# Kernel optimization log

Measured on AMD Instinct MI355X. Metric: run time of the kernel, lower is better.

The kernel has to match this reference:

```python
import jax, jax.numpy as jnp
import numpy as np
from jax import lax

N, C, H, W = 6, 64, 128, 128
BN_EPS = 1e-5


def setup_inputs() -> dict:
    key = jax.random.key(0)
    ks = jax.random.split(key, 16)
    def p(i, shape, scale=0.05):
        return jax.random.normal(ks[i], shape, jnp.float32) * scale
    return {
        "raw_feat": jax.random.normal(ks[0], (N, C, H, W), jnp.float32),
        # PixelWeightedFusionSoftmax params (1x1 convs stored as [out,in] matrices)
        "pw_w1": p(1, (4, C)), "pw_b1": p(2, (4,)),
        "bn_gamma": 1.0 + p(3, (4,)), "bn_beta": p(4, (4,)),
        "bn_mean": jnp.zeros((4,), jnp.float32), "bn_var": jnp.ones((4,), jnp.float32),
        "pw_w2": p(5, (1, 4)), "pw_b2": p(6, (1,)),
        # ConvMod params: a = dwconv11x11(gelu(conv1x1_{2C->C}(q))); out = proj(a * v(v) * att_map)
        "cm_a1_w": p(7, (C, 2 * C)), "cm_a1_b": p(8, (C,)),
        "cm_dw_w": p(9, (C, 1, 11, 11)), "cm_dw_b": p(10, (C,)),
        "cm_v_w": p(11, (C, C)), "cm_v_b": p(12, (C,)),
        "cm_proj_w": p(13, (C, C)), "cm_proj_b": p(14, (C,)),
    }


def _conf_maps(x, pw_w1, pw_b1, bn_gamma, bn_beta, bn_mean, bn_var, pw_w2, pw_b2):
    # x: [N,C,H,W] -> per-agent confidence maps [N,1,H,W], min-max normalized per agent
    h = jnp.einsum('nchw,oc->nohw', x, pw_w1) + pw_b1[:, None, None]
    scale = (bn_gamma / jnp.sqrt(bn_var + BN_EPS))[:, None, None]
    h = (h - bn_mean[:, None, None]) * scale + bn_beta[:, None, None]  # BN eval mode
    h = jax.nn.relu(h)
    h = jax.nn.relu(jnp.einsum('nchw,oc->nohw', h, pw_w2) + pw_b2[:, None, None])
    mn = h.min(axis=(1, 2, 3), keepdims=True)
    mx = h.max(axis=(1, 2, 3), keepdims=True)
    return (h - mn) / (mx - mn)


def reference(raw_feat, pw_w1, pw_b1, bn_gamma, bn_beta, bn_mean, bn_var, pw_w2, pw_b2,
              cm_a1_w, cm_a1_b, cm_dw_w, cm_dw_b, cm_v_w, cm_v_b, cm_proj_w, cm_proj_b):
    conf = _conf_maps(raw_feat, pw_w1, pw_b1, bn_gamma, bn_beta, bn_mean, bn_var, pw_w2, pw_b2)  # [N,1,H,W]
    # att_map[i,k] = (1 - conf_i) * conf_k
    att_map = (1.0 - conf)[:, None] * conf[None, :]  # [N,N,1,H,W]
    # q[i,k] = concat(raw[i], raw[k]) along channels -> [N,N,2C,H,W]
    q = jnp.concatenate([jnp.broadcast_to(raw_feat[:, None], (N, N, C, H, W)),
                         jnp.broadcast_to(raw_feat[None, :], (N, N, C, H, W))], axis=2)
    a = jax.nn.gelu(jnp.einsum('ikchw,oc->ikohw', q, cm_a1_w) + cm_a1_b[:, None, None],
                    approximate=False)
    a = lax.conv_general_dilated(a.reshape(N * N, C, H, W), cm_dw_w,
                                 window_strides=(1, 1), padding='SAME',
                                 feature_group_count=C,
                                 dimension_numbers=('NCHW', 'OIHW', 'NCHW'))
    a = a.reshape(N, N, C, H, W) + cm_dw_b[:, None, None]
    vproj = jnp.einsum('nchw,oc->nohw', raw_feat, cm_v_w) + cm_v_b[:, None, None]  # [N,C,H,W]
    x = a * vproj[None] * att_map  # [N,N,C,H,W]
    out = jnp.einsum('ikchw,oc->ikohw', x, cm_proj_w) + cm_proj_b[:, None, None]
    updated = raw_feat + out.sum(axis=1)  # ego i accumulates over all senders k
    return updated.reshape(N * C, H, W)   # matches torch.cat(local_com_mat_update, dim=0)
```

## Files before the change

kernel.cpp:

```cpp
#include <hip/hip_runtime.h>
#include <hip/hip_fp16.h>
#include <math.h>

#define NAG 6
#define CC  64
#define HH  128
#define WW  128
#define HWT 16384
#define HWP 8192
#define BN_EPS 1e-5f
#define WFRAG_PJ_OFF (24 * 64 * 8)

typedef unsigned int u32;
typedef __fp16 f16x2v __attribute__((ext_vector_type(2)));
typedef __fp16 f16x8  __attribute__((ext_vector_type(8)));
typedef float  f32x4  __attribute__((ext_vector_type(4)));

__device__ __forceinline__ u32 gelu_pk(u32 xu) {
    __half2 x = __builtin_bit_cast(__half2, xu);
    __half2 s = __hmul2(x, x);
    __half2 m = __hfma2(s, __float2half2_rn(-0.10294535f),
                        __float2half2_rn(-2.30226045f));
    __half2 e = h2exp2(__hmul2(x, m));
    __half2 r = h2rcp(__hadd2(e, __float2half2_rn(1.0f)));
    return __builtin_bit_cast(u32, __hmul2(x, r));
}

__global__ __launch_bounds__(256) void k_setup(
    const float* __restrict__ a1w, const float* __restrict__ vw,
    const float* __restrict__ pjw, __fp16* __restrict__ wfrag,
    u32* __restrict__ mm)
{
    int t = blockIdx.x * 256 + threadIdx.x;
    if (t < NAG) mm[t] = 0x7F800000u;
    else if (t < 2 * NAG && t >= NAG) mm[t] = 0u;
    if (t >= 32 * 64) return;
    int lane = t & 63;
    int slot = t >> 6;
    bool pj = slot >= 24;
    int s = pj ? slot - 24 : slot;
    int ot = s >> 1, kf = s & 1;
    int o  = (pj ? ot : (ot & 3)) * 16 + (lane & 15);
    int ch = kf * 32 + (lane >> 4) * 8;
    const float* src;
    if (pj)          src = pjw + o * CC + ch;
    else if (ot < 4) src = a1w + o * 2 * CC + ch;
    else if (ot < 8) src = a1w + o * 2 * CC + CC + ch;
    else             src = vw  + o * CC + ch;
    __fp16* dst = wfrag + ((size_t)slot * 64 + lane) * 8;
    #pragma unroll
    for (int j = 0; j < 8; ++j) dst[j] = (__fp16)src[j];
}

__global__ __launch_bounds__(256) void k_conf(
    const float* __restrict__ raw,
    const float* __restrict__ w1, const float* __restrict__ b1,
    const float* __restrict__ gamma, const float* __restrict__ beta,
    const float* __restrict__ mean, const float* __restrict__ var,
    const float* __restrict__ w2, const float* __restrict__ b2,
    float* __restrict__ conf, u32* __restrict__ mm)
{
    const int n = blockIdx.y;
    const int p = blockIdx.x * 256 + threadIdx.x;
    const float* x = raw + (size_t)(n * CC) * HWT + p;

    float a[4] = {0.f, 0.f, 0.f, 0.f};
    #pragma unroll 8
    for (int c = 0; c < CC; ++c) {
        float v = x[c * HWT];
        a[0] = fmaf(w1[0 * CC + c], v, a[0]);
        a[1] = fmaf(w1[1 * CC + c], v, a[1]);
        a[2] = fmaf(w1[2 * CC + c], v, a[2]);
        a[3] = fmaf(w1[3 * CC + c], v, a[3]);
    }
    float h2 = b2[0];
    #pragma unroll
    for (int o = 0; o < 4; ++o) {
        float sc = gamma[o] * rsqrtf(var[o] + BN_EPS);
        float hb = (a[o] + b1[o] - mean[o]) * sc + beta[o];
        hb = fmaxf(hb, 0.f);
        h2 = fmaf(w2[o], hb, h2);
    }
    h2 = fmaxf(h2, 0.f);
    conf[n * HWT + p] = h2;

    float mn = h2, mx = h2;
    #pragma unroll
    for (int off = 32; off > 0; off >>= 1) {
        mn = fminf(mn, __shfl_xor(mn, off, 64));
        mx = fmaxf(mx, __shfl_xor(mx, off, 64));
    }
    __shared__ float smn[4], smx[4];
    int wid = threadIdx.x >> 6, lane = threadIdx.x & 63;
    if (lane == 0) { smn[wid] = mn; smx[wid] = mx; }
    __syncthreads();
    if (threadIdx.x == 0) {
        mn = fminf(fminf(smn[0], smn[1]), fminf(smn[2], smn[3]));
        mx = fmaxf(fmaxf(smx[0], smx[1]), fmaxf(smx[2], smx[3]));
        atomicMin(&mm[n], __float_as_uint(mn));
        atomicMax(&mm[n + NAG], __float_as_uint(mx));
    }
}

__global__ __launch_bounds__(256) void k_pqv(
    const float* __restrict__ raw, const __fp16* __restrict__ wfrag,
    const float* __restrict__ vb, const float* __restrict__ conf,
    const u32* __restrict__ mm,
    u32* __restrict__ Ph, u32* __restrict__ Qh, u32* __restrict__ Wh)
{
    const int n   = blockIdx.y;
    const int px0 = blockIdx.x * 128;
    const int t = threadIdx.x, lane = t & 63, wv = t >> 6;
    const int lm = lane & 15, kg = lane >> 4;
    const int pxw = px0 + wv * 32;
    const int pxl = pxw + lm;
    const int pxs = pxw + kg * 4;

    const float* rawn = raw + (size_t)n * CC * HWT;

    f16x8 afr[2][2];
    #pragma unroll
    for (int mt = 0; mt < 2; ++mt) {
        #pragma unroll
        for (int kf = 0; kf < 2; ++kf) {
            const float* base = rawn + (size_t)(kf * 32 + kg * 8) * HWT + pxl + mt * 16;
            f16x8 a;
            #pragma unroll
            for (int p = 0; p < 4; ++p) {
                f16x2v h = __builtin_amdgcn_cvt_pkrtz(base[(2 * p) * HWT],
                                                      base[(2 * p + 1) * HWT]);
                a[2 * p] = h.x; a[2 * p + 1] = h.y;
            }
            afr[mt][kf] = a;
        }
    }

    const float mn = __uint_as_float(mm[n]);
    const float mx = __uint_as_float(mm[n + NAG]);
    const float inv = 1.f / (mx - mn);
    f32x4 cn[2];
    #pragma unroll
    for (int mt = 0; mt < 2; ++mt) {
        f32x4 cv = *(const f32x4*)(conf + n * HWT + pxs + mt * 16);
        cn[mt] = (cv - mn) * inv;
    }

    #pragma unroll
    for (int ot = 0; ot < 12; ++ot) {
        f16x8 b0 = *(const f16x8*)(wfrag + ((size_t)(ot * 2 + 0) * 64 + lane) * 8);
        f16x8 b1 = *(const f16x8*)(wfrag + ((size_t)(ot * 2 + 1) * 64 + lane) * 8);
        const int o = (ot & 3) * 16 + lm;
        #pragma unroll
        for (int mt = 0; mt < 2; ++mt) {
            f32x4 acc = (f32x4){0.f, 0.f, 0.f, 0.f};
            acc = __builtin_amdgcn_mfma_f32_16x16x32_f16(afr[mt][0], b0, acc, 0, 0, 0);
            acc = __builtin_amdgcn_mfma_f32_16x16x32_f16(afr[mt][1], b1, acc, 0, 0, 0);
            const int pxb = pxs + mt * 16;
            f32x4 r;
            u32* plane;
            if (ot < 8) {
                r = acc;
                plane = (ot < 4 ? Ph : Qh) + (size_t)(n * CC + o) * HWP + (pxb >> 1);
            } else {
                r = (acc + vb[o]) * cn[mt];
                plane = Wh + (size_t)(n * CC + o) * HWP + (pxb >> 1);
            }
            f16x2v h0 = __builtin_amdgcn_cvt_pkrtz(r[0], r[1]);
            f16x2v h1 = __builtin_amdgcn_cvt_pkrtz(r[2], r[3]);
            *(uint2*)plane = make_uint2(__builtin_bit_cast(u32, h0),
                                        __builtin_bit_cast(u32, h1));
        }
    }
}

#define GPITCH 88
#define GROWS  74
#define GDW    (GROWS * GPITCH / 2)
#define NU2    13

__global__ __launch_bounds__(256, 3) void k_main(
    const u32* __restrict__ Ph, const u32* __restrict__ Qh,
    const u32* __restrict__ Wh, const float* __restrict__ conf,
    const u32* __restrict__ mm,
    const float* __restrict__ a1b, const float* __restrict__ dww,
    const float* __restrict__ dwb, u32* __restrict__ Sh)
{
    const int tile = blockIdx.x;
    const int c    = blockIdx.y;
    const int i    = blockIdx.z;
    const int y0 = (tile >> 1) * 64;
    const int x0 = (tile & 1) * 64;
    const int t    = threadIdx.x;
    const int lane = t & 63;
    const int ty   = t >> 6;
    const int lm   = lane & 15;
    const int kg   = lane >> 4;
    const int kg8  = kg * 8;

    __shared__ __align__(16) u32 GT32[2 * GDW];

    const float bdw = dwb[c];
    const float ba1 = a1b[c];

    const float* wc = dww + c * 121;
    f16x8 afrag[11];
    #pragma unroll
    for (int dy = 0; dy < 11; ++dy) {
        f16x8 a;
        #pragma unroll
        for (int j = 0; j < 8; ++j) {
            int d = kg8 + j - lm - 3;
            int dcl = min(max(d, 0), 10);
            float wv = wc[dy * 11 + dcl];
            a[j] = (__fp16)((d == dcl) ? wv : 0.f);
        }
        afrag[dy] = a;
    }

    f16x2v bias2; bias2.x = (__fp16)ba1; bias2.y = (__fp16)ba1;

    int offs[NU2];
    u32 preg[NU2];
    const u32* Pc = Ph + (size_t)(i * CC + c) * HWP;
    #pragma unroll
    for (int u = 0; u < NU2; ++u) {
        int d = t + u * 256;
        int row = d / (GPITCH / 2);
        int cp  = d - row * (GPITCH / 2);
        int gy = y0 + row - 5;
        int gx = x0 + 2 * cp - 8;
        bool inb = (d < GDW) && (gy >= 0) && (gy < HH) && (gx >= 0) && (gx < WW);
        offs[u] = inb ? (gy * (WW / 2) + (gx >> 1)) : -1;
        u32 p = 0u;
        if (inb) {
            f16x2v ph = __builtin_bit_cast(f16x2v, Pc[offs[u]]) + bias2;
            p = __builtin_bit_cast(u32, ph);
        }
        preg[u] = p;
    }

    const int oy  = y0 + ty * 16 + lm;
    const int obx = x0 + kg * 4;
    const int obase = oy * WW + obx;
    const int rowb = (ty * 16 + lm) * GPITCH + kg8;

    f32x4 sacc[4];
    #pragma unroll
    for (int tx = 0; tx < 4; ++tx) sacc[tx] = (f32x4){0.f, 0.f, 0.f, 0.f};

    u32 qreg[NU2];
    {
        const u32* Qc = Qh + (size_t)(0 * CC + c) * HWP;
        #pragma unroll
        for (int u = 0; u < NU2; ++u)
            qreg[u] = (offs[u] >= 0) ? Qc[offs[u]] : 0u;
    }
    #pragma unroll
    for (int u = 0; u < NU2; ++u) {
        int d = t + u * 256;
        if (u < NU2 - 1 || d < GDW) {
            f16x2v s = __builtin_bit_cast(f16x2v, preg[u]) +
                       __builtin_bit_cast(f16x2v, qreg[u]);
            GT32[d] = gelu_pk(__builtin_bit_cast(u32, s));
        }
    }
    {
        const u32* Qc = Qh + (size_t)(1 * CC + c) * HWP;
        #pragma unroll
        for (int u = 0; u < NU2; ++u)
            qreg[u] = (offs[u] >= 0) ? Qc[offs[u]] : 0u;
    }
    __syncthreads();

    #pragma unroll 1
    for (int k = 0; k < NAG; ++k) {
        const __fp16* GTh = (const __fp16*)(GT32 + (k & 1) * GDW);
        u32* GW = GT32 + ((k + 1) & 1) * GDW;
        const bool dog = (k + 1 < NAG);
        const bool doq = (k + 2 < NAG);
        const u32* Qc2 = Qh + (size_t)((doq ? k + 2 : 0) * CC + c) * HWP;
        const u32* Wc  = Wh + (size_t)(k * CC + c) * HWP + (obase >> 1);

        #pragma unroll
        for (int tx = 0; tx < 4; ++tx) {
            uint2 wvt = *(const uint2*)(Wc + 8 * tx);
            f32x4 acc = (f32x4){0.f, 0.f, 0.f, 0.f};
            __builtin_amdgcn_s_setprio(1);
            #pragma unroll
            for (int dy = 0; dy < 11; ++dy) {
                f16x8 b = *(const f16x8*)(GTh + rowb + dy * GPITCH + 16 * tx);
                acc = __builtin_amdgcn_mfma_f32_16x16x32_f16(afrag[dy], b, acc, 0, 0, 0);
            }
            __builtin_amdgcn_s_setprio(0);
            f16x2v w0 = __builtin_bit_cast(f16x2v, wvt.x);
            f16x2v w1 = __builtin_bit_cast(f16x2v, wvt.y);
            f32x4 wf = (f32x4){(float)w0.x, (float)w0.y, (float)w1.x, (float)w1.y};
            sacc[tx] += (acc + bdw) * wf;

            if (dog) {
                const int u0 = (tx == 3) ? 9 : tx * 3;
                const int u1 = (tx == 3) ? NU2 : tx * 3 + 3;
                #pragma unroll
                for (int u = u0; u < u1; ++u) {
                    int d = t + u * 256;
                    if (u < NU2 - 1 || d < GDW) {
                        f16x2v s = __builtin_bit_cast(f16x2v, preg[u]) +
                                   __builtin_bit_cast(f16x2v, qreg[u]);
                        GW[d] = gelu_pk(__builtin_bit_cast(u32, s));
                        if (doq) qreg[u] = (offs[u] >= 0) ? Qc2[offs[u]] : 0u;
                    }
                }
            }
        }

        if (dog) __syncthreads();
    }

    const float mn = __uint_as_float(mm[i]);
    const float mx = __uint_as_float(mm[i + NAG]);
    const float inv = 1.f / (mx - mn);
    const float* cfi = conf + i * HWT + obase;
    u32* Sc = Sh + (size_t)(i * CC + c) * HWP + (obase >> 1);
    #pragma unroll
    for (int tx = 0; tx < 4; ++tx) {
        f32x4 cv = *(const f32x4*)(cfi + 16 * tx);
        f32x4 r = sacc[tx] * (1.f - (cv - mn) * inv);
        f16x2v h0 = __builtin_amdgcn_cvt_pkrtz(r[0], r[1]);
        f16x2v h1 = __builtin_amdgcn_cvt_pkrtz(r[2], r[3]);
        *(uint2*)(Sc + 8 * tx) = make_uint2(__builtin_bit_cast(u32, h0),
                                            __builtin_bit_cast(u32, h1));
    }
}

__global__ __launch_bounds__(256) void k_out(
    const u32* __restrict__ Sh, const float* __restrict__ raw,
    const __fp16* __restrict__ wfrag, const float* __restrict__ pb,
    float* __restrict__ out)
{
    const int n   = blockIdx.y;
    const int px0 = blockIdx.x * 128;
    const int t = threadIdx.x, lane = t & 63, wv = t >> 6;
    const int lm = lane & 15, kg = lane >> 4;
    const int pxw = px0 + wv * 32;
    const int pxl = pxw + lm;
    const int pxs = pxw + kg * 4;

    const u32* Sn = Sh + (size_t)n * CC * HWP;
    const u32 sh = (pxl & 1) * 16;

    f16x8 afr[2][2];
    #pragma unroll
    for (int mt = 0; mt < 2; ++mt) {
        #pragma unroll
        for (int kf = 0; kf < 2; ++kf) {
            const u32* base = Sn + (size_t)(kf * 32 + kg * 8) * HWP + ((pxl + mt * 16) >> 1);
            f16x8 a;
            #pragma unroll
            for (int j = 0; j < 8; ++j) {
                unsigned short v = (unsigned short)(base[(size_t)j * HWP] >> sh);
                a[j] = __builtin_bit_cast(__fp16, v);
            }
            afr[mt][kf] = a;
        }
    }

    #pragma unroll
    for (int ot = 0; ot < 4; ++ot) {
        f16x8 b0 = *(const f16x8*)(wfrag + WFRAG_PJ_OFF +
                                   ((size_t)(ot * 2 + 0) * 64 + lane) * 8);
        f16x8 b1 = *(const f16x8*)(wfrag + WFRAG_PJ_OFF +
                                   ((size_t)(ot * 2 + 1) * 64 + lane) * 8);
        const int o = ot * 16 + lm;
        const float bias = (float)NAG * pb[o];
        #pragma unroll
        for (int mt = 0; mt < 2; ++mt) {
            f32x4 acc = (f32x4){0.f, 0.f, 0.f, 0.f};
            acc = __builtin_amdgcn_mfma_f32_16x16x32_f16(afr[mt][0], b0, acc, 0, 0, 0);
            acc = __builtin_amdgcn_mfma_f32_16x16x32_f16(afr[mt][1], b1, acc, 0, 0, 0);
            const int pxb = pxs + mt * 16;
            f32x4 r = *(const f32x4*)(raw + (size_t)(n * CC + o) * HWT + pxb);
            f32x4 ov = r + acc + bias;
            *(f32x4*)(out + (size_t)(n * CC + o) * HWT + pxb) = ov;
        }
    }
}

extern "C" void kernel_launch(void* const* d_in, const int* in_sizes, int n_in,
                              void* d_out, int out_size, void* d_ws, size_t ws_size,
                              hipStream_t stream)
{
    (void)in_sizes; (void)n_in; (void)out_size; (void)ws_size;

    const float* raw   = (const float*)d_in[0];
    const float* pw_w1 = (const float*)d_in[1];
    const float* pw_b1 = (const float*)d_in[2];
    const float* bng   = (const float*)d_in[3];
    const float* bnb   = (const float*)d_in[4];
    const float* bnm   = (const float*)d_in[5];
    const float* bnv   = (const float*)d_in[6];
    const float* pw_w2 = (const float*)d_in[7];
    const float* pw_b2 = (const float*)d_in[8];
    const float* a1w   = (const float*)d_in[9];
    const float* a1b   = (const float*)d_in[10];
    const float* dww   = (const float*)d_in[11];
    const float* dwb   = (const float*)d_in[12];
    const float* vw    = (const float*)d_in[13];
    const float* vb    = (const float*)d_in[14];
    const float* pjw   = (const float*)d_in[15];
    const float* pjb   = (const float*)d_in[16];

    float* ws   = (float*)d_ws;
    float* conf = ws;
    u32*   mm   = (u32*)(ws + NAG * HWT);
    u32*   Ph   = (u32*)(ws + NAG * HWT + 16);
    u32*   Qh   = Ph + (size_t)NAG * CC * HWP;
    u32*   Wh   = Qh + (size_t)NAG * CC * HWP;
    u32*   Sh   = Wh + (size_t)NAG * CC * HWP;
    __fp16* wfrag = (__fp16*)(Sh + (size_t)NAG * CC * HWP);
    float* out  = (float*)d_out;

    k_setup<<<dim3(8), dim3(256), 0, stream>>>(a1w, vw, pjw, wfrag, mm);
    k_conf<<<dim3(HWT / 256, NAG), dim3(256), 0, stream>>>(raw, pw_w1, pw_b1, bng, bnb,
                                                           bnm, bnv, pw_w2, pw_b2, conf, mm);
    k_pqv<<<dim3(HWT / 128, NAG), dim3(256), 0, stream>>>(raw, wfrag, vb, conf, mm,
                                                          Ph, Qh, Wh);
    k_main<<<dim3(4, CC, NAG), dim3(256), 0, stream>>>(Ph, Qh, Wh, conf, mm, a1b, dww, dwb, Sh);
    k_out<<<dim3(HWT / 128, NAG), dim3(256), 0, stream>>>(Sh, raw, wfrag, pjb, out);
}
```

Baseline: 105.4 us.

## Fuse confidence-map kernel into projection kernel and defer normalization to main

The separate k_conf pass is removed. Confidence maps are now computed inside the PQV projection kernel from the fp16 activation fragments it already holds in registers, using packed fp16 dot products and cross-lane shuffles. Because the global min/max is not known until every block finishes, the per-agent normalization moves out of W projection and into k_main, which reads conf and scales it there. This saves one full read of raw_feat and one kernel launch, but adds per-iteration conf loads and arithmetic in the main kernel and computes conf with fp16 inputs.

```diff
diff --git a/kernel.cpp b/kernel.cpp
--- a/kernel.cpp
+++ b/kernel.cpp
@@ -10,6 +10,7 @@
 #define HWP 8192
 #define BN_EPS 1e-5f
 #define WFRAG_PJ_OFF (24 * 64 * 8)
+#define WFRAG_W1_OFF (32 * 64 * 8)
 
 typedef unsigned int u32;
 typedef __fp16 f16x2v __attribute__((ext_vector_type(2)));
@@ -26,14 +27,35 @@
     return __builtin_bit_cast(u32, __hmul2(x, r));
 }
 
+__device__ __forceinline__ float dot8(f16x8 a, f16x8 b, float acc) {
+    uint4 au = __builtin_bit_cast(uint4, a);
+    uint4 bu = __builtin_bit_cast(uint4, b);
+    acc = __builtin_amdgcn_fdot2(__builtin_bit_cast(f16x2v, au.x),
+                                 __builtin_bit_cast(f16x2v, bu.x), acc, false);
+    acc = __builtin_amdgcn_fdot2(__builtin_bit_cast(f16x2v, au.y),
+                                 __builtin_bit_cast(f16x2v, bu.y), acc, false);
+    acc = __builtin_amdgcn_fdot2(__builtin_bit_cast(f16x2v, au.z),
+                                 __builtin_bit_cast(f16x2v, bu.z), acc, false);
+    acc = __builtin_amdgcn_fdot2(__builtin_bit_cast(f16x2v, au.w),
+                                 __builtin_bit_cast(f16x2v, bu.w), acc, false);
+    return acc;
+}
+
 __global__ __launch_bounds__(256) void k_setup(
     const float* __restrict__ a1w, const float* __restrict__ vw,
-    const float* __restrict__ pjw, __fp16* __restrict__ wfrag,
-    u32* __restrict__ mm)
+    const float* __restrict__ pjw, const float* __restrict__ w1,
+    __fp16* __restrict__ wfrag, u32* __restrict__ mm)
 {
     int t = blockIdx.x * 256 + threadIdx.x;
     if (t < NAG) mm[t] = 0x7F800000u;
-    else if (t < 2 * NAG && t >= NAG) mm[t] = 0u;
+    else if (t < 2 * NAG) mm[t] = 0u;
+    if (t < 32) {
+        int kf = t >> 4, kg = (t >> 2) & 3, o = t & 3;
+        const float* src = w1 + o * CC + kf * 32 + kg * 8;
+        __fp16* dst = wfrag + WFRAG_W1_OFF + t * 8;
+        #pragma unroll
+        for (int j = 0; j < 8; ++j) dst[j] = (__fp16)src[j];
+    }
     if (t >= 32 * 64) return;
     int lane = t & 63;
     int slot = t >> 6;
@@ -52,60 +74,14 @@
     for (int j = 0; j < 8; ++j) dst[j] = (__fp16)src[j];
 }
 
-__global__ __launch_bounds__(256) void k_conf(
-    const float* __restrict__ raw,
-    const float* __restrict__ w1, const float* __restrict__ b1,
-    const float* __restrict__ gamma, const float* __restrict__ beta,
-    const float* __restrict__ mean, const float* __restrict__ var,
-    const float* __restrict__ w2, const float* __restrict__ b2,
-    float* __restrict__ conf, u32* __restrict__ mm)
-{
-    const int n = blockIdx.y;
-    const int p = blockIdx.x * 256 + threadIdx.x;
-    const float* x = raw + (size_t)(n * CC) * HWT + p;
-
-    float a[4] = {0.f, 0.f, 0.f, 0.f};
-    #pragma unroll 8
-    for (int c = 0; c < CC; ++c) {
-        float v = x[c * HWT];
-        a[0] = fmaf(w1[0 * CC + c], v, a[0]);
-        a[1] = fmaf(w1[1 * CC + c], v, a[1]);
-        a[2] = fmaf(w1[2 * CC + c], v, a[2]);
-        a[3] = fmaf(w1[3 * CC + c], v, a[3]);
-    }
-    float h2 = b2[0];
-    #pragma unroll
-    for (int o = 0; o < 4; ++o) {
-        float sc = gamma[o] * rsqrtf(var[o] + BN_EPS);
-        float hb = (a[o] + b1[o] - mean[o]) * sc + beta[o];
-        hb = fmaxf(hb, 0.f);
-        h2 = fmaf(w2[o], hb, h2);
-    }
-    h2 = fmaxf(h2, 0.f);
-    conf[n * HWT + p] = h2;
-
-    float mn = h2, mx = h2;
-    #pragma unroll
-    for (int off = 32; off > 0; off >>= 1) {
-        mn = fminf(mn, __shfl_xor(mn, off, 64));
-        mx = fmaxf(mx, __shfl_xor(mx, off, 64));
-    }
-    __shared__ float smn[4], smx[4];
-    int wid = threadIdx.x >> 6, lane = threadIdx.x & 63;
-    if (lane == 0) { smn[wid] = mn; smx[wid] = mx; }
-    __syncthreads();
-    if (threadIdx.x == 0) {
-        mn = fminf(fminf(smn[0], smn[1]), fminf(smn[2], smn[3]));
-        mx = fmaxf(fmaxf(smx[0], smx[1]), fmaxf(smx[2], smx[3]));
-        atomicMin(&mm[n], __float_as_uint(mn));
-        atomicMax(&mm[n + NAG], __float_as_uint(mx));
-    }
-}
-
-__global__ __launch_bounds__(256) void k_pqv(
+__global__ __launch_bounds__(256) void k_front(
     const float* __restrict__ raw, const __fp16* __restrict__ wfrag,
-    const float* __restrict__ vb, const float* __restrict__ conf,
-    const u32* __restrict__ mm,
+    const float* __restrict__ vb,
+    const float* __restrict__ b1, const float* __restrict__ gamma,
+    const float* __restrict__ beta, const float* __restrict__ mean,
+    const float* __restrict__ var, const float* __restrict__ w2,
+    const float* __restrict__ b2,
+    float* __restrict__ conf, u32* __restrict__ mm,
     u32* __restrict__ Ph, u32* __restrict__ Qh, u32* __restrict__ Wh)
 {
     const int n   = blockIdx.y;
@@ -135,26 +111,67 @@
         }
     }
 
-    const float mn = __uint_as_float(mm[n]);
-    const float mx = __uint_as_float(mm[n + NAG]);
-    const float inv = 1.f / (mx - mn);
-    f32x4 cn[2];
-    #pragma unroll
-    for (int mt = 0; mt < 2; ++mt) {
-        f32x4 cv = *(const f32x4*)(conf + n * HWT + pxs + mt * 16);
-        cn[mt] = (cv - mn) * inv;
+    float h2v[2];
+    {
+        f16x8 w1v[2][4];
+        #pragma unroll
+        for (int kf = 0; kf < 2; ++kf)
+            #pragma unroll
+            for (int o = 0; o < 4; ++o)
+                w1v[kf][o] = *(const f16x8*)(wfrag + WFRAG_W1_OFF +
+                                             ((kf * 4 + kg) * 4 + o) * 8);
+        #pragma unroll
+        for (int mt = 0; mt < 2; ++mt) {
+            float h1[4];
+            #pragma unroll
+            for (int o = 0; o < 4; ++o) {
+                float a = dot8(w1v[0][o], afr[mt][0], 0.f);
+                a = dot8(w1v[1][o], afr[mt][1], a);
+                a += __shfl_xor(a, 16, 64);
+                a += __shfl_xor(a, 32, 64);
+                h1[o] = a;
+            }
+            float h2 = b2[0];
+            #pragma unroll
+            for (int o = 0; o < 4; ++o) {
+                float sc = gamma[o] * rsqrtf(var[o] + BN_EPS);
+                float hb = (h1[o] + b1[o] - mean[o]) * sc + beta[o];
+                hb = fmaxf(hb, 0.f);
+                h2 = fmaf(w2[o], hb, h2);
+            }
+            h2v[mt] = fmaxf(h2, 0.f);
+        }
+        if (kg == 0) {
+            conf[n * HWT + pxl]      = h2v[0];
+            conf[n * HWT + pxl + 16] = h2v[1];
+        }
+        float mn = fminf(h2v[0], h2v[1]), mx = fmaxf(h2v[0], h2v[1]);
+        #pragma unroll
+        for (int off = 32; off > 0; off >>= 1) {
+            mn = fminf(mn, __shfl_xor(mn, off, 64));
+            mx = fmaxf(mx, __shfl_xor(mx, off, 64));
+        }
+        __shared__ float smn[4], smx[4];
+        if (lane == 0) { smn[wv] = mn; smx[wv] = mx; }
+        __syncthreads();
+        if (t == 0) {
+            mn = fminf(fminf(smn[0], smn[1]), fminf(smn[2], smn[3]));
+            mx = fmaxf(fmaxf(smx[0], smx[1]), fmaxf(smx[2], smx[3]));
+            atomicMin(&mm[n], __float_as_uint(mn));
+            atomicMax(&mm[n + NAG], __float_as_uint(mx));
+        }
     }
 
     #pragma unroll
     for (int ot = 0; ot < 12; ++ot) {
         f16x8 b0 = *(const f16x8*)(wfrag + ((size_t)(ot * 2 + 0) * 64 + lane) * 8);
-        f16x8 b1 = *(const f16x8*)(wfrag + ((size_t)(ot * 2 + 1) * 64 + lane) * 8);
+        f16x8 b1f = *(const f16x8*)(wfrag + ((size_t)(ot * 2 + 1) * 64 + lane) * 8);
         const int o = (ot & 3) * 16 + lm;
         #pragma unroll
         for (int mt = 0; mt < 2; ++mt) {
             f32x4 acc = (f32x4){0.f, 0.f, 0.f, 0.f};
             acc = __builtin_amdgcn_mfma_f32_16x16x32_f16(afr[mt][0], b0, acc, 0, 0, 0);
-            acc = __builtin_amdgcn_mfma_f32_16x16x32_f16(afr[mt][1], b1, acc, 0, 0, 0);
+            acc = __builtin_amdgcn_mfma_f32_16x16x32_f16(afr[mt][1], b1f, acc, 0, 0, 0);
             const int pxb = pxs + mt * 16;
             f32x4 r;
             u32* plane;
@@ -162,7 +179,7 @@
                 r = acc;
                 plane = (ot < 4 ? Ph : Qh) + (size_t)(n * CC + o) * HWP + (pxb >> 1);
             } else {
-                r = (acc + vb[o]) * cn[mt];
+                r = acc + vb[o];
                 plane = Wh + (size_t)(n * CC + o) * HWP + (pxb >> 1);
             }
             f16x2v h0 = __builtin_amdgcn_cvt_pkrtz(r[0], r[1]);
@@ -280,10 +297,16 @@
         const bool doq = (k + 2 < NAG);
         const u32* Qc2 = Qh + (size_t)((doq ? k + 2 : 0) * CC + c) * HWP;
         const u32* Wc  = Wh + (size_t)(k * CC + c) * HWP + (obase >> 1);
+        const float* cfk = conf + (size_t)k * HWT + obase;
+
+        const float mnk = __uint_as_float(mm[k]);
+        const float mxk = __uint_as_float(mm[k + NAG]);
+        const float invk = 1.f / (mxk - mnk);
 
         #pragma unroll
         for (int tx = 0; tx < 4; ++tx) {
             uint2 wvt = *(const uint2*)(Wc + 8 * tx);
+            f32x4 cf4 = *(const f32x4*)(cfk + 16 * tx);
             f32x4 acc = (f32x4){0.f, 0.f, 0.f, 0.f};
             __builtin_amdgcn_s_setprio(1);
             #pragma unroll
@@ -295,6 +318,7 @@
             f16x2v w0 = __builtin_bit_cast(f16x2v, wvt.x);
             f16x2v w1 = __builtin_bit_cast(f16x2v, wvt.y);
             f32x4 wf = (f32x4){(float)w0.x, (float)w0.y, (float)w1.x, (float)w1.y};
+            wf *= (cf4 - mnk) * invk;
             sacc[tx] += (acc + bdw) * wf;
 
             if (dog) {
@@ -419,11 +443,10 @@
     __fp16* wfrag = (__fp16*)(Sh + (size_t)NAG * CC * HWP);
     float* out  = (float*)d_out;
 
-    k_setup<<<dim3(8), dim3(256), 0, stream>>>(a1w, vw, pjw, wfrag, mm);
-    k_conf<<<dim3(HWT / 256, NAG), dim3(256), 0, stream>>>(raw, pw_w1, pw_b1, bng, bnb,
-                                                           bnm, bnv, pw_w2, pw_b2, conf, mm);
-    k_pqv<<<dim3(HWT / 128, NAG), dim3(256), 0, stream>>>(raw, wfrag, vb, conf, mm,
-                                                          Ph, Qh, Wh);
+    k_setup<<<dim3(8), dim3(256), 0, stream>>>(a1w, vw, pjw, pw_w1, wfrag, mm);
+    k_front<<<dim3(HWT / 128, NAG), dim3(256), 0, stream>>>(
+        raw, wfrag, vb, pw_b1, bng, bnb, bnm, bnv, pw_w2, pw_b2,
+        conf, mm, Ph, Qh, Wh);
     k_main<<<dim3(4, CC, NAG), dim3(256), 0, stream>>>(Ph, Qh, Wh, conf, mm, a1b, dww, dwb, Sh);
     k_out<<<dim3(HWT / 128, NAG), dim3(256), 0, stream>>>(Sh, raw, wfrag, pjb, out);
 }
```

Result: slower. 111.8 us (+6.0%).
